# Performance work log

Measured on AMD Instinct MI355X. Metric: run time of the kernel, lower is better.

The kernel has to match this reference:

```python
import jax, jax.numpy as jnp
import numpy as np

EPS = 1e-12  # matches F.normalize default eps


def _l2norm(a, axis):
    n = jnp.sqrt(jnp.sum(a * a, axis=axis, keepdims=True))
    return a / jnp.maximum(n, EPS)


def setup_inputs() -> dict:
    key = jax.random.key(0)
    k1, k2, k3, k4, k5 = jax.random.split(key, 5)
    B, H, W = 512, 64, 64
    Y, Z = 32768, 1000
    x = jax.random.normal(k1, (B, H, W), dtype=jnp.float32)
    z = jax.random.randint(k2, (B,), 0, Z, dtype=jnp.int64 if jax.config.jax_enable_x64 else jnp.int32).astype(jnp.int32)
    x2y_w = jax.random.uniform(k3, (Y, H * W), dtype=jnp.float32)
    y2z_w = jax.random.uniform(k4, (Z, Y), dtype=jnp.float32)
    y_age = jax.random.randint(k5, (1, Y), 0, 3, dtype=jnp.int32)
    return {"x": x, "z": z, "x2y_w": x2y_w, "y2z_w": y2z_w, "y_age": y_age, "per_item": 1}


def reference(x, z, x2y_w, y2z_w, y_age, per_item):
    # DN.forward, mode='test'
    B = x.shape[0]
    Y = x2y_w.shape[0]
    xf = _l2norm(x.reshape(B, -1), axis=1)              # [B, X]
    w_xy = _l2norm(x2y_w, axis=1)                       # row-normalized [Y, X]
    w_yz = _l2norm(y2z_w, axis=1)                       # row-normalized [Z, Y]
    y_bu = jnp.einsum('bx,yx->by', xf, w_xy)            # bottom-up response [B, Y]
    active = (y_age >= 1).astype(y_bu.dtype)            # [1, Y] age gate
    y_pre = y_bu * active                               # gated responses
    # top_k_competition(flag=0): top-1 winner-take-all -> one-hot response
    winner = jnp.argmax(y_pre, axis=1)                  # [B]
    y_resp = jax.nn.one_hot(winner, Y, dtype=y_pre.dtype)  # [B, Y]
    out = jnp.einsum('by,zy->bz', y_resp, w_yz)         # [B, Z]
    return out
```

## Files before the change

### kernel.cpp

```cpp
#include <hip/hip_runtime.h>
#include <math.h>


typedef _Float16 half8 __attribute__((ext_vector_type(8)));
typedef __attribute__((ext_vector_type(16))) float f32x16;
typedef float f32x4 __attribute__((ext_vector_type(4)));
typedef unsigned long long ull;

#define TAU 0.006f
#define CAP 1572864u
#define LCAP 1536u

__device__ __forceinline__ unsigned pk2h(float a, float b) {
    union { _Float16 h; unsigned short u; } ca, cb;
    ca.h = (_Float16)a; cb.h = (_Float16)b;
    return (unsigned)ca.u | ((unsigned)cb.u << 16);
}

__device__ __forceinline__ ull packkey(float v, unsigned y) {
    unsigned m = __float_as_uint(v);
    m = (v >= 0.f) ? (m | 0x80000000u) : ~m;
    return ((ull)m << 32) | (ull)(0x7FFFFFFFu - y);
}

__global__ __launch_bounds__(512) void init_ctrl(const int* __restrict__ age,
                                                 ull* __restrict__ win,
                                                 unsigned* __restrict__ cnt) {
    const int t = threadIdx.x;
    int fi = 0x7fffffff;
    for (int y = t; y < 32768; y += 512)
        if (age[y] < 1) fi = min(fi, y);
    __shared__ int red[512];
    red[t] = fi;
    __syncthreads();
    for (int s = 256; s; s >>= 1) {
        if (t < s) red[t] = min(red[t], red[t + s]);
        __syncthreads();
    }
    const int f = red[0];
    const ull seed = (f < 32768) ? packkey(0.0f, (unsigned)f) : packkey(-1e30f, 0u);
    win[t] = seed;
    if (t == 0) *cnt = 0u;
}

__global__ __launch_bounds__(512) void convert_x(const float* __restrict__ x,
                                                 uint4* __restrict__ xf16) {
    const int o = blockIdx.x * 512 + threadIdx.x;
    const int lane = o & 63;
    const int ks = (o >> 6) & 1;
    const int mi = (o >> 7) & 1;
    const int wm = (o >> 8) & 7;
    const int t  = o >> 11;
    const int row = (wm << 6) + (mi << 5) + (lane & 31);
    const int col = (t << 5) + (ks << 4) + ((lane >> 5) << 3);
    const float* src = x + (size_t)row * 4096 + col;
    const float4 a = *(const float4*)src;
    const float4 b = *(const float4*)(src + 4);
    uint4 u;
    u.x = pk2h(a.x, a.y); u.y = pk2h(a.z, a.w);
    u.z = pk2h(b.x, b.y); u.w = pk2h(b.z, b.w);
    xf16[o] = u;
}

__global__ __launch_bounds__(256) void row_norms(const float* __restrict__ src,
                                                 float* __restrict__ dst, int cols) {
    const int r = blockIdx.x;
    const float* row = src + (size_t)r * cols;
    const int t = threadIdx.x;
    float s = 0.f;
    const int nIter = cols >> 10;
    for (int i = 0; i < nIter; ++i) {
        const float4 v = *reinterpret_cast<const float4*>(row + (((i << 8) + t) << 2));
        s = fmaf(v.x, v.x, s); s = fmaf(v.y, v.y, s);
        s = fmaf(v.z, v.z, s); s = fmaf(v.w, v.w, s);
    }
    #pragma unroll
    for (int off = 32; off; off >>= 1) s += __shfl_down(s, off);
    __shared__ float red[4];
    if ((t & 63) == 0) red[t >> 6] = s;
    __syncthreads();
    if (t == 0) dst[r] = sqrtf(red[0] + red[1] + red[2] + red[3]);
}

__global__ __launch_bounds__(512, 2) void gemm_f16(
    const float* __restrict__ w,
    const uint4* __restrict__ xf16,
    const int*  __restrict__ age,
    float* __restrict__ cand,
    float2* __restrict__ ent,
    unsigned* __restrict__ cnt)
{
    __shared__ uint4 Bl[2][512];
    __shared__ float ny_inv[128];
    __shared__ float rowmaxs[512];
    __shared__ float2 lent[LCAP];
    __shared__ unsigned lcnt, gbase;

    const int tid = threadIdx.x;
    const int y0 = blockIdx.x << 7;

    const int rB = tid >> 2, q = tid & 3;
    const int wiB = (rB << 2) + (q ^ (rB & 3));
    const float* bP = w + (size_t)(y0 + rB) * 4096 + (q << 3);

    const int lane = tid & 63, wm = tid >> 6;
    const int kh = lane >> 5, cc = lane & 3;
    const uint4* aP = xf16 + (wm << 8) + lane;

    const int rb0 = ((lane & 31)      ) << 2;
    const int rb1 = ((lane & 31) +  32) << 2;
    const int rb2 = ((lane & 31) +  64) << 2;
    const int rb3 = ((lane & 31) +  96) << 2;
    const int s0 = kh ^ cc, s1 = (2 | kh) ^ cc;

    f32x16 am0n0 = (f32x16)0.f, am0n1 = (f32x16)0.f;
    f32x16 am0n2 = (f32x16)0.f, am0n3 = (f32x16)0.f;
    f32x16 am1n0 = (f32x16)0.f, am1n1 = (f32x16)0.f;
    f32x16 am1n2 = (f32x16)0.f, am1n3 = (f32x16)0.f;

    half8 pa00, pa01, pa10, pa11;
    half8 qa00, qa01, qa10, qa11;
    half8 g00, g10, g20, g30;
    half8 g01, g11, g21, g31;
    f32x4 SAa, SAb;
    f32x4 SBa, SBb;
    float nyacc = 0.f;

#define MF(a, b, c) __builtin_amdgcn_mfma_f32_32x32x16_f16(a, b, c, 0, 0, 0)
#define LG0 asm volatile("s_waitcnt lgkmcnt(0)" ::: "memory")
#define SBR __builtin_amdgcn_sched_barrier(0)

#define LOADA(S, tt) { const uint4* p_ = aP + ((size_t)(tt) << 11); \
    S##00 = *(const half8*)(p_);        S##01 = *(const half8*)(p_ + 64); \
    S##10 = *(const half8*)(p_ + 128);  S##11 = *(const half8*)(p_ + 192); }

#define LOADW(S, tt) { const f32x4* p_ = (const f32x4*)(bP + ((tt) << 5)); \
    S##a = __builtin_nontemporal_load(p_); \
    S##b = __builtin_nontemporal_load(p_ + 1); }

#define STOREB(buf, S) { uint4 u_; \
    u_.x = pk2h(S##a.x, S##a.y); u_.y = pk2h(S##a.z, S##a.w); \
    u_.z = pk2h(S##b.x, S##b.y); u_.w = pk2h(S##b.z, S##b.w); \
    Bl[buf][wiB] = u_; \
    nyacc = fmaf(S##a.x, S##a.x, nyacc); nyacc = fmaf(S##a.y, S##a.y, nyacc); \
    nyacc = fmaf(S##a.z, S##a.z, nyacc); nyacc = fmaf(S##a.w, S##a.w, nyacc); \
    nyacc = fmaf(S##b.x, S##b.x, nyacc); nyacc = fmaf(S##b.y, S##b.y, nyacc); \
    nyacc = fmaf(S##b.z, S##b.z, nyacc); nyacc = fmaf(S##b.w, S##b.w, nyacc); }

#define LDB(cur) { \
    g00 = *(const half8*)&Bl[cur][rb0 + s0]; g01 = *(const half8*)&Bl[cur][rb0 + s1]; \
    g10 = *(const half8*)&Bl[cur][rb1 + s0]; g11 = *(const half8*)&Bl[cur][rb1 + s1]; \
    g20 = *(const half8*)&Bl[cur][rb2 + s0]; g21 = *(const half8*)&Bl[cur][rb2 + s1]; \
    g30 = *(const half8*)&Bl[cur][rb3 + s0]; g31 = *(const half8*)&Bl[cur][rb3 + s1]; }

#define MFMA16(S) { \
    am0n0 = MF(S##00, g00, am0n0); am0n1 = MF(S##00, g10, am0n1); \
    am0n2 = MF(S##00, g20, am0n2); am0n3 = MF(S##00, g30, am0n3); \
    am1n0 = MF(S##10, g00, am1n0); am1n1 = MF(S##10, g10, am1n1); \
    am1n2 = MF(S##10, g20, am1n2); am1n3 = MF(S##10, g30, am1n3); \
    am0n0 = MF(S##01, g01, am0n0); am0n1 = MF(S##01, g11, am0n1); \
    am0n2 = MF(S##01, g21, am0n2); am0n3 = MF(S##01, g31, am0n3); \
    am1n0 = MF(S##11, g01, am1n0); am1n1 = MF(S##11, g11, am1n1); \
    am1n2 = MF(S##11, g21, am1n2); am1n3 = MF(S##11, g31, am1n3); }

#define TILE(cur, tt, AC, AN, WS, GA, GW) { \
    LDB(cur); \
    if (GA) LOADA(AN, (tt) + 1); \
    if (GA) STOREB((cur) ^ 1, WS); \
    if (GW) LOADW(WS, (tt) + 3); \
    MFMA16(AC); \
    LG0; SBR; \
    __builtin_amdgcn_s_barrier(); }

    LOADW(SA, 0);
    LOADA(pa, 0);
    STOREB(0, SA);
    LOADW(SA, 1);
    LOADW(SB, 2);
    LG0; SBR;
    __builtin_amdgcn_s_barrier();

    for (int t = 0; t < 124; t += 2) {
        TILE(0, t,     pa, qa, SA, 1, 1)
        TILE(1, t + 1, qa, pa, SB, 1, 1)
    }
    TILE(0, 124, pa, qa, SA, 1, 1)
    TILE(1, 125, qa, pa, SB, 1, 0)
    TILE(0, 126, pa, qa, SA, 1, 0)
    TILE(1, 127, qa, pa, SB, 0, 0)

    float s_ = nyacc;
    s_ += __shfl_xor(s_, 1);
    s_ += __shfl_xor(s_, 2);
    if (q == 0) ny_inv[rB] = 1.0f / fmaxf(sqrtf(s_), 1e-12f);
    if (tid == 0) lcnt = 0u;
    __syncthreads();

    const int yl0 = (lane & 31), yl1 = yl0 + 32, yl2 = yl0 + 64, yl3 = yl0 + 96;
    const float scl0 = ny_inv[yl0], scl1 = ny_inv[yl1];
    const float scl2 = ny_inv[yl2], scl3 = ny_inv[yl3];
    const int act0 = age[y0 + yl0] >= 1, act1 = age[y0 + yl1] >= 1;
    const int act2 = age[y0 + yl2] >= 1, act3 = age[y0 + yl3] >= 1;
    const int yb0 = y0 + yl0, yb1 = y0 + yl1, yb2 = y0 + yl2, yb3 = y0 + yl3;
    const int rbase = (wm << 6) + (kh << 2);

#define ROWMAX(A0, A1, A2, A3, mi5) \
    _Pragma("unroll") for (int v = 0; v < 16; ++v) { \
        float bv = fmaxf( \
            fmaxf(act0 ? A0[v] * scl0 : 0.f, act1 ? A1[v] * scl1 : 0.f), \
            fmaxf(act2 ? A2[v] * scl2 : 0.f, act3 ? A3[v] * scl3 : 0.f)); \
        _Pragma("unroll") for (int off = 1; off < 32; off <<= 1) \
            bv = fmaxf(bv, __shfl_xor(bv, off)); \
        if ((lane & 31) == 0) \
            rowmaxs[rbase + (mi5) + (v & 3) + ((v >> 2) << 3)] = bv; \
    }
    ROWMAX(am0n0, am0n1, am0n2, am0n3, 0)
    ROWMAX(am1n0, am1n1, am1n2, am1n3, 32)
    __syncthreads();
    cand[(size_t)tid * 256 + blockIdx.x] = rowmaxs[tid];
    __syncthreads();

#define APP1(ACv, actk, sclk, ybk, r_) { \
    if (actk) { const float sc_ = (ACv) * sclk; \
        if (sc_ >= rowmaxs[r_] - TAU) { \
            const unsigned ix_ = atomicAdd(&lcnt, 1u); \
            if (ix_ < LCAP) lent[ix_] = make_float2(sc_, \
                __uint_as_float(((unsigned)(r_) << 16) | (unsigned)(ybk))); } } }

#define APPEND(A0, A1, A2, A3, mi5) \
    _Pragma("unroll") for (int v = 0; v < 16; ++v) { \
        const int r_ = rbase + (mi5) + (v & 3) + ((v >> 2) << 3); \
        APP1(A0[v], act0, scl0, yb0, r_) \
        APP1(A1[v], act1, scl1, yb1, r_) \
        APP1(A2[v], act2, scl2, yb2, r_) \
        APP1(A3[v], act3, scl3, yb3, r_) }
    APPEND(am0n0, am0n1, am0n2, am0n3, 0)
    APPEND(am1n0, am1n1, am1n2, am1n3, 32)
    __syncthreads();
    if (tid == 0) gbase = atomicAdd(cnt, min(lcnt, LCAP));
    __syncthreads();
    const unsigned nL = min(lcnt, LCAP);
    for (unsigned i = tid; i < nL; i += 512) {
        const unsigned gi = gbase + i;
        if (gi < CAP) ent[gi] = lent[i];
    }
#undef MF
#undef LG0
#undef SBR
#undef LOADA
#undef LOADW
#undef STOREB
#undef LDB
#undef MFMA16
#undef TILE
#undef ROWMAX
#undef APP1
#undef APPEND
}

__global__ __launch_bounds__(256) void reduce_gmax(const float* __restrict__ cand,
                                                   float* __restrict__ gmax) {
    const int b = blockIdx.x, t = threadIdx.x;
    float m = cand[(size_t)b * 256 + t];
    #pragma unroll
    for (int off = 32; off; off >>= 1) m = fmaxf(m, __shfl_xor(m, off));
    __shared__ float sm[4];
    if ((t & 63) == 0) sm[t >> 6] = m;
    __syncthreads();
    if (t == 0) gmax[b] = fmaxf(fmaxf(sm[0], sm[1]), fmaxf(sm[2], sm[3]));
}

__global__ __launch_bounds__(256) void rescore(
    const float* __restrict__ x, const float* __restrict__ w,
    const float* __restrict__ gmax, const float2* __restrict__ ent,
    const unsigned* __restrict__ cnt, ull* __restrict__ win)
{
    const unsigned n = min(*cnt, CAP);
    const int lane = threadIdx.x & 63;
    const unsigned wid = (blockIdx.x * 256 + threadIdx.x) >> 6;
    const unsigned nwv = (gridDim.x * 256) >> 6;
    for (unsigned base = wid << 6; base < n; base += (nwv << 6)) {
        const unsigned e = base + (unsigned)lane;
        unsigned by = 0u;
        bool ok = false;
        if (e < n) {
            const float2 en = ent[e];
            by = __float_as_uint(en.y);
            ok = en.x >= gmax[by >> 16] - TAU;
        }
        ull m = __ballot(ok);
        while (m) {
            const int s = __ffsll((ull)m) - 1;
            m &= m - 1;
            const unsigned bys = __shfl(by, s);
            const unsigned b = bys >> 16, y = bys & 0xffffu;
            const float4* xr = (const float4*)(x + (size_t)b * 4096);
            const float4* wr = (const float4*)(w + (size_t)y * 4096);
            float sdot = 0.f, nn = 0.f;
            #pragma unroll
            for (int k = 0; k < 16; ++k) {
                const float4 xv = xr[(k << 6) + lane];
                const float4 wv = wr[(k << 6) + lane];
                sdot = fmaf(xv.x, wv.x, sdot); sdot = fmaf(xv.y, wv.y, sdot);
                sdot = fmaf(xv.z, wv.z, sdot); sdot = fmaf(xv.w, wv.w, sdot);
                nn = fmaf(wv.x, wv.x, nn); nn = fmaf(wv.y, wv.y, nn);
                nn = fmaf(wv.z, wv.z, nn); nn = fmaf(wv.w, wv.w, nn);
            }
            #pragma unroll
            for (int off = 32; off; off >>= 1) {
                sdot += __shfl_xor(sdot, off);
                nn   += __shfl_xor(nn, off);
            }
            if (lane == 0) {
                const float sc = sdot / fmaxf(sqrtf(nn), 1e-12f);
                atomicMax(win + b, packkey(sc, y));
            }
        }
    }
}

__global__ __launch_bounds__(256) void gather_out(const float* __restrict__ y2z,
                                                  const float* __restrict__ nz,
                                                  const ull* __restrict__ win,
                                                  float* __restrict__ out) {
    const int g = blockIdx.x * 256 + threadIdx.x;
    if (g >= 512 * 1000) return;
    const int b = g / 1000, z = g - b * 1000;
    const unsigned lo = (unsigned)(win[b] & 0xffffffffull);
    const int yw = (int)(0x7FFFFFFFu - lo);
    out[g] = y2z[(size_t)z * 32768 + yw] / fmaxf(nz[z], 1e-12f);
}

extern "C" void kernel_launch(void* const* d_in, const int* in_sizes, int n_in,
                              void* d_out, int out_size, void* d_ws, size_t ws_size,
                              hipStream_t stream) {
    const float* x     = (const float*)d_in[0];
    const float* x2y_w = (const float*)d_in[2];
    const float* y2z_w = (const float*)d_in[3];
    const int*   y_age = (const int*)d_in[4];
    float* out = (float*)d_out;

    char* p = (char*)d_ws;
    float*    cand = (float*)p;
    float*    nz   = (float*)(p + 524288);
    float*    gmax = (float*)(p + 528384);
    ull*      win  = (ull*)(p + 530432);
    unsigned* cnt  = (unsigned*)(p + 534528);
    uint4*    xf16 = (uint4*)(p + 534592);
    float2*   ent  = (float2*)(p + 4728896);

    init_ctrl<<<1, 512, 0, stream>>>(y_age, win, cnt);
    convert_x<<<512, 512, 0, stream>>>(x, xf16);
    row_norms<<<1000, 256, 0, stream>>>(y2z_w, nz, 32768);

    gemm_f16<<<256, 512, 0, stream>>>(x2y_w, xf16, y_age, cand, ent, cnt);
    reduce_gmax<<<512, 256, 0, stream>>>(cand, gmax);
    rescore<<<256, 256, 0, stream>>>(x, x2y_w, gmax, ent, cnt, win);
    gather_out<<<(512 * 1000 + 255) / 256, 256, 0, stream>>>(y2z_w, nz, win, out);
}
```

Before: 263.9 us.

## Halve GEMM block tile to 64 Y columns and double grid for higher occupancy

The f16 MFMA GEMM block now covers 64 Y rows instead of 128, with half the accumulators, B-fragment registers and LDS staging. The grid doubles to 512 blocks, launch bounds ask for 4 blocks per CU, and only the first 256 threads stage weights. The A-operand double buffer is removed, so A is loaded after the MFMAs within each tile and latency hiding moves from that prefetch to extra waves. Each block now reloads the full 512x4096 activation, which doubles activation traffic. The candidate-max buffer widens to 512 columns, with reduce_gmax and the workspace offsets updated to match.

```diff
diff --git a/kernel.cpp b/kernel.cpp
--- a/kernel.cpp
+++ b/kernel.cpp
@@ -9,7 +9,7 @@
 
 #define TAU 0.006f
 #define CAP 1572864u
-#define LCAP 1536u
+#define LCAP 1024u
 
 __device__ __forceinline__ unsigned pk2h(float a, float b) {
     union { _Float16 h; unsigned short u; } ca, cb;
@@ -82,7 +82,7 @@
     if (t == 0) dst[r] = sqrtf(red[0] + red[1] + red[2] + red[3]);
 }
 
-__global__ __launch_bounds__(512, 2) void gemm_f16(
+__global__ __launch_bounds__(512, 4) void gemm_f16(
     const float* __restrict__ w,
     const uint4* __restrict__ xf16,
     const int*  __restrict__ age,
@@ -90,38 +90,33 @@
     float2* __restrict__ ent,
     unsigned* __restrict__ cnt)
 {
-    __shared__ uint4 Bl[2][512];
-    __shared__ float ny_inv[128];
+    __shared__ uint4 Bl[2][256];
+    __shared__ float ny_inv[64];
     __shared__ float rowmaxs[512];
     __shared__ float2 lent[LCAP];
     __shared__ unsigned lcnt, gbase;
 
     const int tid = threadIdx.x;
-    const int y0 = blockIdx.x << 7;
+    const int y0 = blockIdx.x << 6;
 
     const int rB = tid >> 2, q = tid & 3;
     const int wiB = (rB << 2) + (q ^ (rB & 3));
-    const float* bP = w + (size_t)(y0 + rB) * 4096 + (q << 3);
+    const float* bP = w + (size_t)(y0 + (rB & 63)) * 4096 + (q << 3);
+    const int isStager = (tid < 256);
 
     const int lane = tid & 63, wm = tid >> 6;
     const int kh = lane >> 5, cc = lane & 3;
     const uint4* aP = xf16 + (wm << 8) + lane;
 
     const int rb0 = ((lane & 31)      ) << 2;
-    const int rb1 = ((lane & 31) +  32) << 2;
-    const int rb2 = ((lane & 31) +  64) << 2;
-    const int rb3 = ((lane & 31) +  96) << 2;
+    const int rb1 = ((lane & 31) + 32) << 2;
     const int s0 = kh ^ cc, s1 = (2 | kh) ^ cc;
 
     f32x16 am0n0 = (f32x16)0.f, am0n1 = (f32x16)0.f;
-    f32x16 am0n2 = (f32x16)0.f, am0n3 = (f32x16)0.f;
     f32x16 am1n0 = (f32x16)0.f, am1n1 = (f32x16)0.f;
-    f32x16 am1n2 = (f32x16)0.f, am1n3 = (f32x16)0.f;
 
     half8 pa00, pa01, pa10, pa11;
-    half8 qa00, qa01, qa10, qa11;
-    half8 g00, g10, g20, g30;
-    half8 g01, g11, g21, g31;
+    half8 g00, g01, g10, g11;
     f32x4 SAa, SAb;
     f32x4 SBa, SBb;
     float nyacc = 0.f;
@@ -149,75 +144,67 @@
 
 #define LDB(cur) { \
     g00 = *(const half8*)&Bl[cur][rb0 + s0]; g01 = *(const half8*)&Bl[cur][rb0 + s1]; \
-    g10 = *(const half8*)&Bl[cur][rb1 + s0]; g11 = *(const half8*)&Bl[cur][rb1 + s1]; \
-    g20 = *(const half8*)&Bl[cur][rb2 + s0]; g21 = *(const half8*)&Bl[cur][rb2 + s1]; \
-    g30 = *(const half8*)&Bl[cur][rb3 + s0]; g31 = *(const half8*)&Bl[cur][rb3 + s1]; }
-
-#define MFMA16(S) { \
-    am0n0 = MF(S##00, g00, am0n0); am0n1 = MF(S##00, g10, am0n1); \
-    am0n2 = MF(S##00, g20, am0n2); am0n3 = MF(S##00, g30, am0n3); \
-    am1n0 = MF(S##10, g00, am1n0); am1n1 = MF(S##10, g10, am1n1); \
-    am1n2 = MF(S##10, g20, am1n2); am1n3 = MF(S##10, g30, am1n3); \
-    am0n0 = MF(S##01, g01, am0n0); am0n1 = MF(S##01, g11, am0n1); \
-    am0n2 = MF(S##01, g21, am0n2); am0n3 = MF(S##01, g31, am0n3); \
-    am1n0 = MF(S##11, g01, am1n0); am1n1 = MF(S##11, g11, am1n1); \
-    am1n2 = MF(S##11, g21, am1n2); am1n3 = MF(S##11, g31, am1n3); }
-
-#define TILE(cur, tt, AC, AN, WS, GA, GW) { \
+    g10 = *(const half8*)&Bl[cur][rb1 + s0]; g11 = *(const half8*)&Bl[cur][rb1 + s1]; }
+
+#define MFMA8 { \
+    am0n0 = MF(pa00, g00, am0n0); am0n1 = MF(pa00, g10, am0n1); \
+    am1n0 = MF(pa10, g00, am1n0); am1n1 = MF(pa10, g10, am1n1); \
+    am0n0 = MF(pa01, g01, am0n0); am0n1 = MF(pa01, g11, am0n1); \
+    am1n0 = MF(pa11, g01, am1n0); am1n1 = MF(pa11, g11, am1n1); }
+
+#define TILE(cur, tt, WS, GA, GW) { \
     LDB(cur); \
-    if (GA) LOADA(AN, (tt) + 1); \
-    if (GA) STOREB((cur) ^ 1, WS); \
-    if (GW) LOADW(WS, (tt) + 3); \
-    MFMA16(AC); \
+    if (GA && isStager) STOREB((cur) ^ 1, WS); \
+    if (GW && isStager) LOADW(WS, (tt) + 3); \
+    MFMA8; \
+    if (GA) LOADA(pa, (tt) + 1); \
     LG0; SBR; \
     __builtin_amdgcn_s_barrier(); }
 
-    LOADW(SA, 0);
+    if (isStager) {
+        LOADW(SA, 0);
+        STOREB(0, SA);
+        LOADW(SA, 1);
+        LOADW(SB, 2);
+    }
     LOADA(pa, 0);
-    STOREB(0, SA);
-    LOADW(SA, 1);
-    LOADW(SB, 2);
     LG0; SBR;
     __builtin_amdgcn_s_barrier();
 
     for (int t = 0; t < 124; t += 2) {
-        TILE(0, t,     pa, qa, SA, 1, 1)
-        TILE(1, t + 1, qa, pa, SB, 1, 1)
-    }
-    TILE(0, 124, pa, qa, SA, 1, 1)
-    TILE(1, 125, qa, pa, SB, 1, 0)
-    TILE(0, 126, pa, qa, SA, 1, 0)
-    TILE(1, 127, qa, pa, SB, 0, 0)
+        TILE(0, t,     SA, 1, 1)
+        TILE(1, t + 1, SB, 1, 1)
+    }
+    TILE(0, 124, SA, 1, 1)
+    TILE(1, 125, SB, 1, 0)
+    TILE(0, 126, SA, 1, 0)
+    TILE(1, 127, SB, 0, 0)
 
     float s_ = nyacc;
     s_ += __shfl_xor(s_, 1);
     s_ += __shfl_xor(s_, 2);
-    if (q == 0) ny_inv[rB] = 1.0f / fmaxf(sqrtf(s_), 1e-12f);
+    if (isStager && q == 0) ny_inv[rB] = 1.0f / fmaxf(sqrtf(s_), 1e-12f);
     if (tid == 0) lcnt = 0u;
     __syncthreads();
 
-    const int yl0 = (lane & 31), yl1 = yl0 + 32, yl2 = yl0 + 64, yl3 = yl0 + 96;
+    const int yl0 = (lane & 31), yl1 = yl0 + 32;
     const float scl0 = ny_inv[yl0], scl1 = ny_inv[yl1];
-    const float scl2 = ny_inv[yl2], scl3 = ny_inv[yl3];
     const int act0 = age[y0 + yl0] >= 1, act1 = age[y0 + yl1] >= 1;
-    const int act2 = age[y0 + yl2] >= 1, act3 = age[y0 + yl3] >= 1;
-    const int yb0 = y0 + yl0, yb1 = y0 + yl1, yb2 = y0 + yl2, yb3 = y0 + yl3;
+    const int yb0 = y0 + yl0, yb1 = y0 + yl1;
     const int rbase = (wm << 6) + (kh << 2);
 
-#define ROWMAX(A0, A1, A2, A3, mi5) \
+#define ROWMAX(A0, A1, mi5) \
     _Pragma("unroll") for (int v = 0; v < 16; ++v) { \
-        float bv = fmaxf( \
-            fmaxf(act0 ? A0[v] * scl0 : 0.f, act1 ? A1[v] * scl1 : 0.f), \
-            fmaxf(act2 ? A2[v] * scl2 : 0.f, act3 ? A3[v] * scl3 : 0.f)); \
+        float bv = fmaxf(act0 ? A0[v] * scl0 : 0.f, act1 ? A1[v] * scl1 : 0.f); \
         _Pragma("unroll") for (int off = 1; off < 32; off <<= 1) \
             bv = fmaxf(bv, __shfl_xor(bv, off)); \
         if ((lane & 31) == 0) \
             rowmaxs[rbase + (mi5) + (v & 3) + ((v >> 2) << 3)] = bv; \
     }
-    ROWMAX(am0n0, am0n1, am0n2, am0n3, 0)
-    ROWMAX(am1n0, am1n1, am1n2, am1n3, 32)
-    __syncthreads();
-    cand[(size_t)tid * 256 + blockIdx.x] = rowmaxs[tid];
+    ROWMAX(am0n0, am0n1, 0)
+    ROWMAX(am1n0, am1n1, 32)
+    __syncthreads();
+    cand[(size_t)tid * 512 + blockIdx.x] = rowmaxs[tid];
     __syncthreads();
 
 #define APP1(ACv, actk, sclk, ybk, r_) { \
@@ -227,15 +214,13 @@
             if (ix_ < LCAP) lent[ix_] = make_float2(sc_, \
                 __uint_as_float(((unsigned)(r_) << 16) | (unsigned)(ybk))); } } }
 
-#define APPEND(A0, A1, A2, A3, mi5) \
+#define APPEND(A0, A1, mi5) \
     _Pragma("unroll") for (int v = 0; v < 16; ++v) { \
         const int r_ = rbase + (mi5) + (v & 3) + ((v >> 2) << 3); \
         APP1(A0[v], act0, scl0, yb0, r_) \
-        APP1(A1[v], act1, scl1, yb1, r_) \
-        APP1(A2[v], act2, scl2, yb2, r_) \
-        APP1(A3[v], act3, scl3, yb3, r_) }
-    APPEND(am0n0, am0n1, am0n2, am0n3, 0)
-    APPEND(am1n0, am1n1, am1n2, am1n3, 32)
+        APP1(A1[v], act1, scl1, yb1, r_) }
+    APPEND(am0n0, am0n1, 0)
+    APPEND(am1n0, am1n1, 32)
     __syncthreads();
     if (tid == 0) gbase = atomicAdd(cnt, min(lcnt, LCAP));
     __syncthreads();
@@ -251,7 +236,7 @@
 #undef LOADW
 #undef STOREB
 #undef LDB
-#undef MFMA16
+#undef MFMA8
 #undef TILE
 #undef ROWMAX
 #undef APP1
@@ -261,7 +246,7 @@
 __global__ __launch_bounds__(256) void reduce_gmax(const float* __restrict__ cand,
                                                    float* __restrict__ gmax) {
     const int b = blockIdx.x, t = threadIdx.x;
-    float m = cand[(size_t)b * 256 + t];
+    float m = fmaxf(cand[(size_t)b * 512 + t], cand[(size_t)b * 512 + t + 256]);
     #pragma unroll
     for (int off = 32; off; off >>= 1) m = fmaxf(m, __shfl_xor(m, off));
     __shared__ float sm[4];
@@ -342,18 +327,18 @@
 
     char* p = (char*)d_ws;
     float*    cand = (float*)p;
-    float*    nz   = (float*)(p + 524288);
-    float*    gmax = (float*)(p + 528384);
-    ull*      win  = (ull*)(p + 530432);
-    unsigned* cnt  = (unsigned*)(p + 534528);
-    uint4*    xf16 = (uint4*)(p + 534592);
-    float2*   ent  = (float2*)(p + 4728896);
+    float*    nz   = (float*)(p + 1048576);
+    float*    gmax = (float*)(p + 1052672);
+    ull*      win  = (ull*)(p + 1054720);
+    unsigned* cnt  = (unsigned*)(p + 1058816);
+    uint4*    xf16 = (uint4*)(p + 1058880);
+    float2*   ent  = (float2*)(p + 5253184);
 
     init_ctrl<<<1, 512, 0, stream>>>(y_age, win, cnt);
     convert_x<<<512, 512, 0, stream>>>(x, xf16);
     row_norms<<<1000, 256, 0, stream>>>(y2z_w, nz, 32768);
 
-    gemm_f16<<<256, 512, 0, stream>>>(x2y_w, xf16, y_age, cand, ent, cnt);
+    gemm_f16<<<512, 512, 0, stream>>>(x2y_w, xf16, y_age, cand, ent, cnt);
     reduce_gmax<<<512, 256, 0, stream>>>(cand, gmax);
     rescore<<<256, 256, 0, stream>>>(x, x2y_w, gmax, ent, cnt, win);
     gather_out<<<(512 * 1000 + 255) / 256, 256, 0, stream>>>(y2z_w, nz, win, out);
```

Measured after the change: 294.7 us. +11.7%, slower.
